# Performance work log

Hardware: AMD Instinct MI355X
Metric: run time of the kernel (lower is better)

## Reference

```python
import jax, jax.numpy as jnp
import numpy as np

B, C, N, K = 8, 3, 4096, 20
EPS = 1e-5

def bn(x, g, b, axes):
    # training-mode batch norm: normalize over batch/spatial axes, channel last
    m = jnp.mean(x, axes, keepdims=True)
    v = jnp.var(x, axes, keepdims=True)
    return g * (x - m) * jax.lax.rsqrt(v + EPS) + b

def setup_inputs() -> dict:
    key = jax.random.key(0)
    ks = jax.random.split(key, 8)
    def xav(kk, shape):
        fan_out, fan_in = shape
        lim = (6.0 / (fan_in + fan_out)) ** 0.5
        return jax.random.uniform(kk, shape, minval=-lim, maxval=lim, dtype=jnp.float32)
    return dict(
        x=jax.random.normal(ks[0], (B, C, N), dtype=jnp.float32),
        w1=xav(ks[1], (64, 2 * C)), g1=jnp.ones(64), b1=jnp.zeros(64),
        w2=xav(ks[2], (128, 64)), g2=jnp.ones(128), b2=jnp.zeros(128),
        w3=xav(ks[3], (1024, 128)), g3=jnp.ones(1024), b3=jnp.zeros(1024),
        w4=xav(ks[4], (512, 1024)), g4=jnp.ones(512), b4=jnp.zeros(512),
        w5=xav(ks[5], (256, 512)), g5=jnp.ones(256), b5=jnp.zeros(256),
        wl=jnp.zeros((9, 256), dtype=jnp.float32),  # zero-init per reset_parameters
        bl=jnp.zeros(9, dtype=jnp.float32),
    )

def reference(x, w1, g1, b1, w2, g2, b2, w3, g3, b3, w4, g4, b4, w5, g5, b5, wl, bl):
    xt = jnp.transpose(x, (0, 2, 1))  # (B, N, C)
    sq = jnp.sum(xt * xt, -1)  # (B, N)
    # negative squared pairwise distance: -(|a|^2 - 2ab + |b|^2)
    nd = 2.0 * jnp.einsum('bnc,bmc->bnm', xt, xt) - sq[:, :, None] - sq[:, None, :]
    _, idx = jax.lax.top_k(nd, K)  # (B, N, K) nearest neighbors (includes self)
    nbr = jax.vmap(lambda pts, ids: pts[ids])(xt, idx)  # (B, N, K, C)
    ctr = xt[:, :, None, :]
    edge = jnp.concatenate([jnp.broadcast_to(ctr, (B, N, K, C)), nbr - ctr], -1)  # (B,N,K,2C)
    # EdgeConv shared MLP (1x1 conv + BN + ReLU), then max over k
    h = jax.nn.relu(bn(jnp.einsum('bnkc,oc->bnko', edge, w1), g1, b1, (0, 1, 2)))
    h = jax.nn.relu(bn(jnp.einsum('bnkc,oc->bnko', h, w2), g2, b2, (0, 1, 2)))
    h = jnp.max(h, 2)  # (B, N, 128)
    # local shared MLP then global max pool over points
    h = jax.nn.relu(bn(jnp.einsum('bnc,oc->bno', h, w3), g3, b3, (0, 1)))
    h = jnp.max(h, 1)  # (B, 1024)
    # global MLP
    h = jax.nn.relu(bn(h @ w4.T, g4, b4, (0,)))
    h = jax.nn.relu(bn(h @ w5.T, g5, b5, (0,)))
    y = (h @ wl.T + bl).reshape(B, 3, 3)
    return y + jnp.eye(3, dtype=y.dtype)
```

## Files before the change

### kernel.cpp

```cpp
#include <hip/hip_runtime.h>

#define NPTS 4096
#define KNN 20
#define CNT1f 655360.0f
#define CNT3f 32768.0f
#define BNEPS 1e-5f

#define OFF_IDX   0
#define OFF_M     655360
#define OFF_ES    655360
#define OFF_G1P   656384
#define OFF_S1P   672768
#define ZERO1_BEG 655360
#define ZERO1_CNT 17664
#define OFF_W2B   2752512
#define OFF_W3B   2756608
#define OFF_XP    2822144
#define OFF_G3P   2953216
#define OFF_SM3P  2985984
#define OFF_GMAX  2986240
#define OFF_Z4    2994432
#define ZG3_BEG   2953216
#define ZG3_CNT   41216
#define OFF_SC1   4849664
#define OFF_SH1   4849728
#define OFF_SC2   4849792
#define OFF_SH2   4849920
#define OFF_SC3   4850048
#define OFF_SH3   4851072

typedef float f32x4 __attribute__((ext_vector_type(4)));
typedef short s16x8 __attribute__((ext_vector_type(8)));

__device__ __forceinline__ unsigned short f2bf(float f) {
    unsigned u = __float_as_uint(f);
    return (unsigned short)((u + 0x7FFFu + ((u >> 16) & 1u)) >> 16);
}

__global__ __launch_bounds__(256) void k_initprep(const float* __restrict__ x,
                                                  const float* __restrict__ w2,
                                                  const float* __restrict__ w3, float* W) {
    int i = blockIdx.x * 256 + threadIdx.x;
    unsigned short* w2b = (unsigned short*)(W + OFF_W2B);
    unsigned short* w3b = (unsigned short*)(W + OFF_W3B);
    w3b[i] = f2bf(w3[i]);
    if (i < 8192) w2b[i] = f2bf(w2[i]);
    if (i < ZERO1_CNT) W[ZERO1_BEG + i] = 0.0f;
    if (i < ZG3_CNT) W[ZG3_BEG + i] = 0.0f;
    if (i < 32768) {
        int b = i >> 12, j = i & 4095;
        float4 p;
        p.x = x[b * 12288 + j];
        p.y = x[b * 12288 + 4096 + j];
        p.z = x[b * 12288 + 8192 + j];
        p.w = 0.f;
        ((float4*)(W + OFF_XP))[i] = p;
    }
}

template <int PER>
__device__ __forceinline__ void wave_scan_find(const int* H, int K, int lane,
                                               int& B, int& below, int& hB) {
    int c[PER]; int s = 0;
    const int base = lane * PER;
#pragma unroll
    for (int p = 0; p < PER; ++p) { c[p] = H[base + p]; s += c[p]; }
    int pre = s;
#pragma unroll
    for (int off = 1; off < 64; off <<= 1) {
        int t = __shfl_up(pre, off, 64);
        if (lane >= off) pre += t;
    }
    int excl = pre - s;
    bool has = (excl < K) && (K <= excl + s);
    unsigned long long m = __ballot(has);
    int src = (int)(__ffsll((unsigned long long)m) - 1);
    int mb = 0, mbelow = 0, mh = 0;
    if (lane == src) {
        int cum = excl;
#pragma unroll
        for (int p = 0; p < PER; ++p) {
            if (cum < K && K <= cum + c[p]) { mb = base + p; mbelow = cum; mh = c[p]; break; }
            cum += c[p];
        }
    }
    B = __shfl(mb, src, 64);
    below = __shfl(mbelow, src, 64);
    hB = __shfl(mh, src, 64);
}

__global__ __launch_bounds__(256) void k_knn(int* __restrict__ idx, float* W) {
    __shared__ int hist[4][1024];
    __shared__ int outi[4][20];
    __shared__ int cnts[4][2];
    __shared__ float estat[27];
    const int tid = threadIdx.x;
    const int b = blockIdx.y;
    const float4* xb4 = ((const float4*)(W + OFF_XP)) + b * NPTS;
    if (tid < 27) estat[tid] = 0.f;
    if (tid < 8) cnts[tid >> 1][tid & 1] = 0;
    const int wv = tid >> 6, lane = tid & 63;
    const int q = blockIdx.x * 4 + wv;
    const float4 qp = xb4[q];
    int* H = hist[wv];
    unsigned int key[64];
    unsigned int mymin = 0xFFFFFFFFu;
#pragma unroll
    for (int p = 0; p < 16; ++p) H[lane * 16 + p] = 0;
#pragma unroll
    for (int it = 0; it < 64; ++it) {
        int j = it * 64 + lane;
        float4 pp = xb4[j];
        float dx = pp.x - qp.x, dy = pp.y - qp.y, dz = pp.z - qp.z;
        float d = fmaf(dx, dx, fmaf(dy, dy, dz * dz));
        unsigned int u = (j == q) ? 0xFFFFFFFFu : __float_as_uint(d);
        key[it] = u;
        mymin = mymin < u ? mymin : u;
    }
    __syncthreads();
#pragma unroll
    for (int off = 32; off; off >>= 1) {
        unsigned int o = (unsigned int)__shfl_xor((int)mymin, off);
        mymin = mymin < o ? mymin : o;
    }
    const unsigned int base = mymin;
#pragma unroll
    for (int it = 0; it < 64; ++it) {
        unsigned int t9 = key[it] - base;
        unsigned int bin = t9 >> 19; if (bin > 1023u) bin = 1023u;
        atomicAdd(&H[bin], 1);
    }
    int B, below, hB;
    wave_scan_find<16>(H, KNN - 1, lane, B, below, hB);
    unsigned int P = (unsigned int)B;
    int rem = (KNN - 1) - below;
    int S = 19;
    if (hB != rem) {
#pragma unroll
        for (int p = 0; p < 8; ++p) H[lane * 8 + p] = 0;
#pragma unroll
        for (int it = 0; it < 64; ++it) {
            unsigned int t9 = key[it] - base;
            unsigned int b0 = t9 >> 19; if (b0 > 1023u) b0 = 1023u;
            if (b0 == P) atomicAdd(&H[(t9 >> 10) & 511], 1);
        }
        wave_scan_find<8>(H, rem, lane, B, below, hB);
        P = (P << 9) | (unsigned int)B;
        rem -= below;
        S = 10;
        if (hB != rem) {
#pragma unroll
            for (int p = 0; p < 8; ++p) H[lane * 8 + p] = 0;
#pragma unroll
            for (int it = 0; it < 64; ++it) {
                unsigned int t9 = key[it] - base;
                if ((t9 >> 10) == P) atomicAdd(&H[(t9 >> 1) & 511], 1);
            }
            wave_scan_find<8>(H, rem, lane, B, below, hB);
            P = (P << 9) | (unsigned int)B;
            rem -= below;
            S = 1;
        }
    }
    int* OC = cnts[wv];
#pragma unroll
    for (int it = 0; it < 64; ++it) {
        unsigned int t9 = key[it] - base;
        unsigned int v;
        if (S == 19) { v = t9 >> 19; if (v > 1023u) v = 1023u; }
        else v = t9 >> S;
        if (v <= P) {
            bool take = v < P;
            if (!take) { int e = atomicAdd(&OC[1], 1); take = (e < rem); }
            if (take) { int pos = atomicAdd(&OC[0], 1); outi[wv][pos] = it * 64 + lane; }
        }
    }
    if (lane == 0) outi[wv][KNN - 1] = q;
    const int obase = (b * NPTS + q) * KNN;
    if (lane < KNN) idx[obase + lane] = outi[wv][lane];
    float st[27];
#pragma unroll
    for (int v = 0; v < 27; ++v) st[v] = 0.f;
    if (lane < KNN) {
        int j = outi[wv][lane];
        float4 np = xb4[j];
        float e[6];
        e[0] = qp.x; e[1] = qp.y; e[2] = qp.z;
        e[3] = np.x - qp.x; e[4] = np.y - qp.y; e[5] = np.z - qp.z;
        int id = 6;
#pragma unroll
        for (int i = 0; i < 6; ++i) {
            st[i] = e[i];
#pragma unroll
            for (int jj = i; jj < 6; ++jj) { st[id] = e[i] * e[jj]; id++; }
        }
    }
#pragma unroll
    for (int v = 0; v < 27; ++v) {
        float s = st[v];
        s += __shfl_xor(s, 32); s += __shfl_xor(s, 16); s += __shfl_xor(s, 8);
        s += __shfl_xor(s, 4);  s += __shfl_xor(s, 2);  s += __shfl_xor(s, 1);
        st[v] = s;
    }
    if (lane == 0) {
#pragma unroll
        for (int v = 0; v < 27; ++v) atomicAdd(&estat[v], st[v]);
    }
    __syncthreads();
    if (tid < 27) atomicAdd(&W[OFF_ES + (blockIdx.x & 31) * 32 + tid], estat[tid]);
}

__global__ void k_fin1(const float* __restrict__ w1, const float* __restrict__ g1,
                       const float* __restrict__ b1, float* W) {
    __shared__ float es[27];
    const int c = threadIdx.x;
    if (c < 27) {
        float s = 0.f;
        for (int p = 0; p < 32; ++p) s += W[OFF_ES + p * 32 + c];
        es[c] = s;
    }
    __syncthreads();
    float wr[6];
#pragma unroll
    for (int i = 0; i < 6; ++i) wr[i] = w1[c * 6 + i];
    float m = 0.f;
#pragma unroll
    for (int i = 0; i < 6; ++i) m += wr[i] * es[i];
    m *= (1.f / CNT1f);
    float qv = 0.f;
    int id = 6;
#pragma unroll
    for (int i = 0; i < 6; ++i)
#pragma unroll
        for (int jj = 0; jj < 6; ++jj)
            if (jj >= i) { qv += (jj == i ? 1.f : 2.f) * wr[i] * wr[jj] * es[id]; id++; }
    qv *= (1.f / CNT1f);
    float var = qv - m * m;
    float sc = g1[c] * rsqrtf(var + BNEPS);
    W[OFF_SC1 + c] = sc;
    W[OFF_SH1 + c] = b1[c] - m * sc;
}

__global__ __launch_bounds__(256) void k_gram1(const int* __restrict__ idx,
                                               const float* __restrict__ w1, float* W) {
    __shared__ unsigned short h1t[80 * 136];
    __shared__ float eds[128 * 6];
    __shared__ float w1s[64 * 6];
    __shared__ float sc1s[64], sh1s[64];
    const int t = threadIdx.x;
    const int b = blockIdx.x >> 6;
    const int ebase_b = (blockIdx.x & 63) * 1280;
    const float4* xpb = ((const float4*)(W + OFF_XP)) + b * NPTS;
    if (t < 384) w1s[t] = w1[t];
    if (t < 64) { sc1s[t] = W[OFF_SC1 + t]; sh1s[t] = W[OFF_SH1 + t]; }
    for (int i = t; i < 2048; i += 256) {
        int rr = i >> 7, e = i & 127;
        h1t[(64 + rr) * 136 + e] = (rr == 0) ? (unsigned short)0x3F80 : (unsigned short)0;
    }
    const int w = t >> 6, lane = t & 63, n16 = lane & 15, quad = lane >> 4;
    f32x4 acc[5];
#pragma unroll
    for (int j = 0; j < 5; ++j) acc[j] = (f32x4){0.f, 0.f, 0.f, 0.f};
    for (int ck = 0; ck < 10; ++ck) {
        __syncthreads();
        if (t < 128) {
            int e_l = ebase_b + ck * 128 + t;
            int q = e_l / KNN;
            int jn = idx[b * (NPTS * KNN) + e_l];
            float4 c = xpb[q];
            float4 n = xpb[jn];
            float* E = &eds[t * 6];
            E[0] = c.x; E[1] = c.y; E[2] = c.z;
            E[3] = n.x - c.x; E[4] = n.y - c.y; E[5] = n.z - c.z;
        }
        __syncthreads();
        {
            const int e128 = t & 127, half = t >> 7;
            float e0 = eds[e128 * 6 + 0], e1 = eds[e128 * 6 + 1], e2 = eds[e128 * 6 + 2];
            float e3 = eds[e128 * 6 + 3], e4 = eds[e128 * 6 + 4], e5 = eds[e128 * 6 + 5];
#pragma unroll 4
            for (int cc = 0; cc < 32; ++cc) {
                int c = half * 32 + cc;
                const float* wr = &w1s[c * 6];
                float z = wr[0] * e0 + wr[1] * e1 + wr[2] * e2 + wr[3] * e3 + wr[4] * e4 + wr[5] * e5;
                float h = sc1s[c] * z + sh1s[c];
                h1t[c * 136 + e128] = f2bf(h > 0.f ? h : 0.f);
            }
        }
        __syncthreads();
#pragma unroll
        for (int ks = 0; ks < 4; ++ks) {
            s16x8 Af = *(const s16x8*)&h1t[(w * 16 + n16) * 136 + ks * 32 + quad * 8];
#pragma unroll
            for (int jt = 0; jt < 5; ++jt) {
                s16x8 Bf = *(const s16x8*)&h1t[(jt * 16 + n16) * 136 + ks * 32 + quad * 8];
                acc[jt] = __builtin_amdgcn_mfma_f32_16x16x32_bf16(Af, Bf, acc[jt], 0, 0, 0);
            }
        }
    }
    const int part = blockIdx.x & 3;
    const int gi = w * 16 + quad * 4;
#pragma unroll
    for (int jt = 0; jt < 4; ++jt)
#pragma unroll
        for (int r = 0; r < 4; ++r)
            atomicAdd(&W[OFF_G1P + part * 4096 + (gi + r) * 64 + jt * 16 + n16], acc[jt][r]);
    if (n16 == 0) {
#pragma unroll
        for (int r = 0; r < 4; ++r)
            atomicAdd(&W[OFF_S1P + part * 64 + gi + r], acc[4][r]);
    }
}

__global__ __launch_bounds__(256) void k_fin2(const float* __restrict__ w2, const float* __restrict__ g2,
                                              const float* __restrict__ b2, float* W) {
    __shared__ float Gs[4096];
    __shared__ float s1s[64];
    __shared__ float w2s[128 * 65];
    const int t = threadIdx.x;
    for (int i = t; i < 4096; i += 256)
        Gs[i] = W[OFF_G1P + i] + W[OFF_G1P + 4096 + i] + W[OFF_G1P + 8192 + i] + W[OFF_G1P + 12288 + i];
    if (t < 64) s1s[t] = W[OFF_S1P + t] + W[OFF_S1P + 64 + t] + W[OFF_S1P + 128 + t] + W[OFF_S1P + 192 + t];
    for (int i = t; i < 8192; i += 256) w2s[(i >> 6) * 65 + (i & 63)] = w2[i];
    __syncthreads();
    const int c = t >> 1, half = t & 1;
    float acc = 0.f;
    for (int ii = 0; ii < 32; ++ii) {
        int i = 32 * half + ii;
        float wi = w2s[c * 65 + i];
        float inner = 0.f;
        for (int j = 0; j < 64; ++j) inner += Gs[i * 64 + j] * w2s[c * 65 + j];
        acc += wi * inner;
    }
    acc += __shfl_xor(acc, 1);
    if (half == 0) {
        float ms = 0.f;
        for (int j = 0; j < 64; ++j) ms += w2s[c * 65 + j] * s1s[j];
        float mean = ms * (1.f / CNT1f);
        float var = acc * (1.f / CNT1f) - mean * mean;
        float sc = g2[c] * rsqrtf(var + BNEPS);
        W[OFF_SC2 + c] = sc;
        W[OFF_SH2 + c] = b2[c] - mean * sc;
    }
}

__global__ __launch_bounds__(256) void k_c2apply(const int* __restrict__ idx,
                                                 const float* __restrict__ w1, float* W) {
    __shared__ unsigned short h1b[256 * 72];
    __shared__ float eds[160 * 6];
    const int t = threadIdx.x;
    const int b = blockIdx.y, q0 = blockIdx.x * 8;
    const float4* xpb = ((const float4*)(W + OFF_XP)) + b * NPTS;
    const int ebase = (b * NPTS + q0) * KNN;
    const unsigned short* w2b = (const unsigned short*)(W + OFF_W2B);
    if (t < 160) {
        int q = q0 + t / KNN;
        int jn = idx[ebase + t];
        float4 c = xpb[q];
        float4 n = xpb[jn];
        float* E = &eds[t * 6];
        E[0] = c.x; E[1] = c.y; E[2] = c.z;
        E[3] = n.x - c.x; E[4] = n.y - c.y; E[5] = n.z - c.z;
    }
    __syncthreads();
    {
        const int j64 = t & 63, grp = t >> 6;
        float wr[6];
#pragma unroll
        for (int i = 0; i < 6; ++i) wr[i] = w1[j64 * 6 + i];
        const float sc = W[OFF_SC1 + j64], sh = W[OFF_SH1 + j64];
        for (int qq = grp * 2; qq < grp * 2 + 2; ++qq) {
#pragma unroll 4
            for (int kk = 0; kk < 32; ++kk) {
                float v = 0.f;
                if (kk < 20) {
                    const float* E = &eds[(qq * 20 + kk) * 6];
                    float z = wr[0] * E[0] + wr[1] * E[1] + wr[2] * E[2] + wr[3] * E[3] + wr[4] * E[4] + wr[5] * E[5];
                    float h = sc * z + sh;
                    v = h > 0.f ? h : 0.f;
                }
                h1b[(qq * 32 + kk) * 72 + j64] = f2bf(v);
            }
        }
    }
    __syncthreads();
    const int w = t >> 6, lane = t & 63, n16 = lane & 15, quad = lane >> 4;
    unsigned short* Mb = (unsigned short*)(W + OFF_M);
#pragma unroll
    for (int nt_i = 0; nt_i < 2; ++nt_i) {
        const int nt = 2 * w + nt_i;
        const int chan = nt * 16 + n16;
        const float sc2 = W[OFF_SC2 + chan], sh2 = W[OFF_SH2 + chan];
        s16x8 Bf0 = *(const s16x8*)&w2b[chan * 64 + quad * 8];
        s16x8 Bf1 = *(const s16x8*)&w2b[chan * 64 + 32 + quad * 8];
#pragma unroll
        for (int q = 0; q < 8; ++q) {
            f32x4 accA = (f32x4){0.f, 0.f, 0.f, 0.f};
            f32x4 accB = (f32x4){0.f, 0.f, 0.f, 0.f};
            s16x8 a0 = *(const s16x8*)&h1b[(q * 32 + n16) * 72 + quad * 8];
            s16x8 a1 = *(const s16x8*)&h1b[(q * 32 + 16 + n16) * 72 + quad * 8];
            accA = __builtin_amdgcn_mfma_f32_16x16x32_bf16(a0, Bf0, accA, 0, 0, 0);
            accB = __builtin_amdgcn_mfma_f32_16x16x32_bf16(a1, Bf0, accB, 0, 0, 0);
            a0 = *(const s16x8*)&h1b[(q * 32 + n16) * 72 + 32 + quad * 8];
            a1 = *(const s16x8*)&h1b[(q * 32 + 16 + n16) * 72 + 32 + quad * 8];
            accA = __builtin_amdgcn_mfma_f32_16x16x32_bf16(a0, Bf1, accA, 0, 0, 0);
            accB = __builtin_amdgcn_mfma_f32_16x16x32_bf16(a1, Bf1, accB, 0, 0, 0);
            float mx = 0.f;
#pragma unroll
            for (int r = 0; r < 4; ++r) {
                float h = sc2 * accA[r] + sh2;
                mx = fmaxf(mx, h > 0.f ? h : 0.f);
            }
            if (quad == 0) {
#pragma unroll
                for (int r = 0; r < 4; ++r) {
                    float h = sc2 * accB[r] + sh2;
                    mx = fmaxf(mx, h > 0.f ? h : 0.f);
                }
            }
            mx = fmaxf(mx, __shfl_xor(mx, 16));
            mx = fmaxf(mx, __shfl_xor(mx, 32));
            if (quad == 0)
                Mb[(b * NPTS + q0 + q) * 128 + chan] = f2bf(mx);
        }
    }
}

__global__ __launch_bounds__(256) void k_gram3(float* W) {
    __shared__ unsigned short Mt[128 * 72];
    const int t = threadIdx.x;
    const int w = t >> 6, lane = t & 63, n16 = lane & 15, quad = lane >> 4;
    const int r0 = blockIdx.x * 512;
    const unsigned int* Msrc = (const unsigned int*)(W + OFF_M);
    const int nA = 8 - w;
    f32x4 acc[9];
#pragma unroll
    for (int j = 0; j < 9; ++j) acc[j] = (f32x4){0.f, 0.f, 0.f, 0.f};
    float smacc = 0.f;
    for (int ch = 0; ch < 8; ++ch) {
        __syncthreads();
        for (int i = t; i < 4096; i += 256) {
            int row = i >> 6, c2 = i & 63;
            unsigned int v = Msrc[(r0 + ch * 64 + row) * 64 + c2];
            Mt[(2 * c2) * 72 + row]     = (unsigned short)(v & 0xFFFFu);
            Mt[(2 * c2 + 1) * 72 + row] = (unsigned short)(v >> 16);
        }
        __syncthreads();
#pragma unroll
        for (int j = 0; j < 9; ++j) {
            int ti = (j < nA) ? w : (7 - w);
            int tj = (j < nA) ? (w + j) : (j - nA + 7 - w);
#pragma unroll
            for (int ks = 0; ks < 2; ++ks) {
                s16x8 Af = *(const s16x8*)&Mt[(ti * 16 + n16) * 72 + ks * 32 + quad * 8];
                s16x8 Bf = *(const s16x8*)&Mt[(tj * 16 + n16) * 72 + ks * 32 + quad * 8];
                acc[j] = __builtin_amdgcn_mfma_f32_16x16x32_bf16(Af, Bf, acc[j], 0, 0, 0);
            }
        }
        if (t < 128) {
            float s = 0.f;
            for (int e = 0; e < 64; ++e)
                s += __uint_as_float((unsigned int)Mt[t * 72 + e] << 16);
            smacc += s;
        }
    }
    const int part = blockIdx.x & 1;
    float* Gp = &W[OFF_G3P + part * 16384];
#pragma unroll
    for (int j = 0; j < 9; ++j) {
        int ti = (j < nA) ? w : (7 - w);
        int tj = (j < nA) ? (w + j) : (j - nA + 7 - w);
#pragma unroll
        for (int r = 0; r < 4; ++r)
            atomicAdd(&Gp[(ti * 16 + quad * 4 + r) * 128 + tj * 16 + n16], acc[j][r]);
    }
    if (t < 128) atomicAdd(&W[OFF_SM3P + part * 128 + t], smacc);
}

__global__ __launch_bounds__(256) void k_fin3(const float* __restrict__ w3, const float* __restrict__ g3,
                                              const float* __restrict__ b3, float* W) {
    __shared__ float G3s[128 * 129];
    __shared__ float w3s[16 * 132];
    __shared__ float sm3[128];
    __shared__ float red[256];
    __shared__ float mred[16];
    const int t = threadIdx.x;
    const int c0 = blockIdx.x * 16;
    for (int i = t; i < 16384; i += 256) {
        int row = i >> 7, col = i & 127;
        int src = ((row >> 4) <= (col >> 4)) ? (row * 128 + col) : (col * 128 + row);
        G3s[row * 129 + col] = W[OFF_G3P + src] + W[OFF_G3P + 16384 + src];
    }
    for (int i = t; i < 2048; i += 256)
        w3s[(i >> 7) * 132 + (i & 127)] = w3[(c0 + (i >> 7)) * 128 + (i & 127)];
    if (t < 128) sm3[t] = W[OFF_SM3P + t] + W[OFF_SM3P + 128 + t];
    __syncthreads();
    const int cl = t >> 4, seg = t & 15;
    float acc = 0.f;
    for (int ii = 0; ii < 8; ++ii) {
        int i = 8 * seg + ii;
        float wi = w3s[cl * 132 + i];
        float inner = 0.f;
        for (int j = 0; j < 128; ++j) inner += G3s[i * 129 + j] * w3s[cl * 132 + j];
        acc += wi * inner;
    }
    red[t] = acc;
    if (seg == 0) {
        float ms = 0.f;
        for (int j = 0; j < 128; ++j) ms += w3s[cl * 132 + j] * sm3[j];
        mred[cl] = ms;
    }
    __syncthreads();
    if (t < 16) {
        float s = 0.f;
#pragma unroll
        for (int k = 0; k < 16; ++k) s += red[t * 16 + k];
        float mean = mred[t] * (1.f / CNT3f);
        float var = s * (1.f / CNT3f) - mean * mean;
        float sc = g3[c0 + t] * rsqrtf(var + BNEPS);
        W[OFF_SC3 + c0 + t] = sc;
        W[OFF_SH3 + c0 + t] = b3[c0 + t] - mean * sc;
    }
}

__global__ __launch_bounds__(256) void k_conv3(float* W) {
    __shared__ unsigned short Mt[64 * 136];
    const int t = threadIdx.x;
    const int p0 = blockIdx.x * 64, c0g = blockIdx.y * 128;
    const unsigned int* Msrc = (const unsigned int*)(W + OFF_M);
    const unsigned short* w3b = (const unsigned short*)(W + OFF_W3B);
    for (int i = t; i < 4096; i += 256) {
        int row = i >> 6, c2 = i & 63;
        *(unsigned int*)&Mt[row * 136 + 2 * c2] = Msrc[(p0 + row) * 64 + c2];
    }
    __syncthreads();
    const int w = t >> 6, lane = t & 63, n16 = lane & 15, quad = lane >> 4;
    const int bbatch = p0 >> 12;
#pragma unroll
    for (int nt_i = 0; nt_i < 2; ++nt_i) {
        const int nt = 2 * w + nt_i;
        const int chan = c0g + nt * 16 + n16;
        const float sc3 = W[OFF_SC3 + chan], sh3 = W[OFF_SH3 + chan];
        s16x8 Bf[4];
#pragma unroll
        for (int ks = 0; ks < 4; ++ks)
            Bf[ks] = *(const s16x8*)&w3b[chan * 128 + ks * 32 + quad * 8];
        float mx = 0.f;
#pragma unroll
        for (int mt = 0; mt < 4; ++mt) {
            f32x4 acc = (f32x4){0.f, 0.f, 0.f, 0.f};
#pragma unroll
            for (int ks = 0; ks < 4; ++ks) {
                s16x8 Af = *(const s16x8*)&Mt[(mt * 16 + n16) * 136 + ks * 32 + quad * 8];
                acc = __builtin_amdgcn_mfma_f32_16x16x32_bf16(Af, Bf[ks], acc, 0, 0, 0);
            }
#pragma unroll
            for (int r = 0; r < 4; ++r) {
                float h = sc3 * acc[r] + sh3;
                mx = fmaxf(mx, h > 0.f ? h : 0.f);
            }
        }
        mx = fmaxf(mx, __shfl_xor(mx, 16));
        mx = fmaxf(mx, __shfl_xor(mx, 32));
        if (quad == 0)
            atomicMax((unsigned int*)&W[OFF_GMAX + bbatch * 1024 + chan], __float_as_uint(mx));
    }
}

__global__ __launch_bounds__(256) void k_fc4(const float* __restrict__ w4, float* W) {
    __shared__ float red[256];
    const int t = threadIdx.x;
    const int oidx = t >> 3, s = t & 7;
    const int cc = oidx >> 3, b = oidx & 7;
    const int c = blockIdx.x * 4 + cc;
    const float* g = &W[OFF_GMAX];
    const float* wr = &w4[c * 1024 + s * 128];
    const float* gr = &g[b * 1024 + s * 128];
    float p = 0.f;
    for (int j = 0; j < 128; ++j) p += wr[j] * gr[j];
    red[t] = p;
    __syncthreads();
    if (t < 32) {
        float tot = 0.f;
        for (int k = 0; k < 8; ++k) tot += red[t * 8 + k];
        W[OFF_Z4 + (t & 7) * 512 + blockIdx.x * 4 + (t >> 3)] = tot;
    }
}

__global__ __launch_bounds__(512) void k_tail(const float* __restrict__ g4, const float* __restrict__ b4,
                                              const float* __restrict__ w5, const float* __restrict__ g5,
                                              const float* __restrict__ b5, const float* __restrict__ wl,
                                              const float* __restrict__ bl, float* W, float* __restrict__ out) {
    __shared__ float h4L[8 * 512];
    __shared__ float w5s[2 * 256 * 9];
    __shared__ float zp[2 * 2048];
    const int t = threadIdx.x;
    {
        float v[8]; float s = 0.f, q = 0.f;
#pragma unroll
        for (int b = 0; b < 8; ++b) { v[b] = W[OFF_Z4 + b * 512 + t]; s += v[b]; q += v[b] * v[b]; }
        float mean = s * 0.125f;
        float var = q * 0.125f - mean * mean;
        float sc = g4[t] * rsqrtf(var + BNEPS);
        float sh = b4[t] - mean * sc;
#pragma unroll
        for (int b = 0; b < 8; ++b) {
            float h = sc * v[b] + sh;
            h4L[b * 512 + t] = h > 0.f ? h : 0.f;
        }
    }
    const int c5 = t & 255, half = t >> 8;
    float acc[8];
#pragma unroll
    for (int b = 0; b < 8; ++b) acc[b] = 0.f;
    for (int jt = 0; jt < 32; ++jt) {
        __syncthreads();
        for (int i = t; i < 4096; i += 512) {
            int h = i >> 11, rem = i & 2047;
            int ci = rem >> 3, jj = rem & 7;
            w5s[h * 2304 + ci * 9 + jj] = w5[ci * 512 + h * 256 + jt * 8 + jj];
        }
        __syncthreads();
#pragma unroll
        for (int jj = 0; jj < 8; ++jj) {
            float wv = w5s[half * 2304 + c5 * 9 + jj];
            int jg = half * 256 + jt * 8 + jj;
#pragma unroll
            for (int b = 0; b < 8; ++b) acc[b] += wv * h4L[b * 512 + jg];
        }
    }
#pragma unroll
    for (int b = 0; b < 8; ++b) zp[half * 2048 + b * 256 + c5] = acc[b];
    __syncthreads();
    if (t < 256) {
        float v[8], s = 0.f, q = 0.f;
#pragma unroll
        for (int b = 0; b < 8; ++b) {
            v[b] = zp[b * 256 + t] + zp[2048 + b * 256 + t];
            s += v[b]; q += v[b] * v[b];
        }
        float mean = s * 0.125f, var = q * 0.125f - mean * mean;
        float sc = g5[t] * rsqrtf(var + BNEPS), sh = b5[t] - mean * sc;
#pragma unroll
        for (int b = 0; b < 8; ++b) { float h = sc * v[b] + sh; zp[b * 256 + t] = h > 0.f ? h : 0.f; }
    }
    __syncthreads();
    if (t < 72) {
        int b = t / 9, r = t % 9;
        float a = bl[r] + ((r == 0 || r == 4 || r == 8) ? 1.f : 0.f);
        for (int j = 0; j < 256; ++j) a += wl[r * 256 + j] * zp[b * 256 + j];
        out[b * 9 + r] = a;
    }
}

extern "C" void kernel_launch(void* const* d_in, const int* in_sizes, int n_in,
                              void* d_out, int out_size, void* d_ws, size_t ws_size,
                              hipStream_t stream) {
    const float* x  = (const float*)d_in[0];
    const float* w1 = (const float*)d_in[1];
    const float* g1 = (const float*)d_in[2];
    const float* b1 = (const float*)d_in[3];
    const float* w2 = (const float*)d_in[4];
    const float* g2 = (const float*)d_in[5];
    const float* b2 = (const float*)d_in[6];
    const float* w3 = (const float*)d_in[7];
    const float* g3 = (const float*)d_in[8];
    const float* b3 = (const float*)d_in[9];
    const float* w4 = (const float*)d_in[10];
    const float* g4 = (const float*)d_in[11];
    const float* b4 = (const float*)d_in[12];
    const float* w5 = (const float*)d_in[13];
    const float* g5 = (const float*)d_in[14];
    const float* b5 = (const float*)d_in[15];
    const float* wl = (const float*)d_in[16];
    const float* bl = (const float*)d_in[17];
    float* W = (float*)d_ws;
    int* idx = (int*)d_ws;
    float* out = (float*)d_out;

    k_initprep<<<dim3(512), dim3(256), 0, stream>>>(x, w2, w3, W);
    k_knn<<<dim3(1024, 8), dim3(256), 0, stream>>>(idx, W);
    k_fin1<<<dim3(1), dim3(64), 0, stream>>>(w1, g1, b1, W);
    k_gram1<<<dim3(512), dim3(256), 0, stream>>>(idx, w1, W);
    k_fin2<<<dim3(1), dim3(256), 0, stream>>>(w2, g2, b2, W);
    k_c2apply<<<dim3(512, 8), dim3(256), 0, stream>>>(idx, w1, W);
    k_gram3<<<dim3(64), dim3(256), 0, stream>>>(W);
    k_fin3<<<dim3(64), dim3(256), 0, stream>>>(w3, g3, b3, W);
    k_conv3<<<dim3(512, 8), dim3(256), 0, stream>>>(W);
    k_fc4<<<dim3(128), dim3(256), 0, stream>>>(w4, W);
    k_tail<<<dim3(1), dim3(512), 0, stream>>>(g4, b4, w5, g5, b5, wl, bl, W, out);
}
```

Measured before the change: 597.0 us.

## Split each kNN query across two waves to halve per-thread key registers

The kNN selection kernel now handles one query with two cooperating waves (128 threads) instead of one wave, so each thread holds 32 distance keys instead of 64. The grid doubles to keep the same number of queries. The radix-select histogram shrinks to 512 bins and always runs three passes with block barriers, dropping the old early exit. The goal is lower register pressure and higher occupancy, at the cost of extra __syncthreads, always doing all passes, and slightly coarser final key resolution for tie handling.

```diff
diff --git a/kernel.cpp b/kernel.cpp
--- a/kernel.cpp
+++ b/kernel.cpp
@@ -90,26 +90,29 @@
 }
 
 __global__ __launch_bounds__(256) void k_knn(int* __restrict__ idx, float* W) {
-    __shared__ int hist[4][1024];
-    __shared__ int outi[4][20];
-    __shared__ int cnts[4][2];
+    __shared__ int hist[2][512];
+    __shared__ int outi[2][20];
+    __shared__ int cnts[2][2];
+    __shared__ unsigned int minsh[2][2];
     __shared__ float estat[27];
     const int tid = threadIdx.x;
     const int b = blockIdx.y;
     const float4* xb4 = ((const float4*)(W + OFF_XP)) + b * NPTS;
     if (tid < 27) estat[tid] = 0.f;
-    if (tid < 8) cnts[tid >> 1][tid & 1] = 0;
+    if (tid < 4) cnts[tid >> 1][tid & 1] = 0;
     const int wv = tid >> 6, lane = tid & 63;
-    const int q = blockIdx.x * 4 + wv;
+    const int pair = wv >> 1, half = wv & 1;
+    const int tid128 = tid & 127;
+    const int q = blockIdx.x * 2 + pair;
     const float4 qp = xb4[q];
-    int* H = hist[wv];
-    unsigned int key[64];
+    int* H = hist[pair];
+#pragma unroll
+    for (int p = 0; p < 4; ++p) H[tid128 * 4 + p] = 0;
+    unsigned int key[32];
     unsigned int mymin = 0xFFFFFFFFu;
 #pragma unroll
-    for (int p = 0; p < 16; ++p) H[lane * 16 + p] = 0;
-#pragma unroll
-    for (int it = 0; it < 64; ++it) {
-        int j = it * 64 + lane;
+    for (int it = 0; it < 32; ++it) {
+        int j = it * 128 + tid128;
         float4 pp = xb4[j];
         float dx = pp.x - qp.x, dy = pp.y - qp.y, dz = pp.z - qp.z;
         float d = fmaf(dx, dx, fmaf(dy, dy, dz * dz));
@@ -117,72 +120,71 @@
         key[it] = u;
         mymin = mymin < u ? mymin : u;
     }
-    __syncthreads();
 #pragma unroll
     for (int off = 32; off; off >>= 1) {
         unsigned int o = (unsigned int)__shfl_xor((int)mymin, off);
         mymin = mymin < o ? mymin : o;
     }
-    const unsigned int base = mymin;
-#pragma unroll
-    for (int it = 0; it < 64; ++it) {
+    if (lane == 0) minsh[pair][half] = mymin;
+    __syncthreads();
+    const unsigned int base = minsh[pair][0] < minsh[pair][1] ? minsh[pair][0] : minsh[pair][1];
+#pragma unroll
+    for (int it = 0; it < 32; ++it) {
         unsigned int t9 = key[it] - base;
-        unsigned int bin = t9 >> 19; if (bin > 1023u) bin = 1023u;
+        unsigned int bin = t9 >> 20; if (bin > 511u) bin = 511u;
         atomicAdd(&H[bin], 1);
     }
+    __syncthreads();
     int B, below, hB;
-    wave_scan_find<16>(H, KNN - 1, lane, B, below, hB);
+    wave_scan_find<8>(H, KNN - 1, lane, B, below, hB);
     unsigned int P = (unsigned int)B;
     int rem = (KNN - 1) - below;
-    int S = 19;
-    if (hB != rem) {
-#pragma unroll
-        for (int p = 0; p < 8; ++p) H[lane * 8 + p] = 0;
-#pragma unroll
-        for (int it = 0; it < 64; ++it) {
-            unsigned int t9 = key[it] - base;
-            unsigned int b0 = t9 >> 19; if (b0 > 1023u) b0 = 1023u;
-            if (b0 == P) atomicAdd(&H[(t9 >> 10) & 511], 1);
-        }
-        wave_scan_find<8>(H, rem, lane, B, below, hB);
-        P = (P << 9) | (unsigned int)B;
-        rem -= below;
-        S = 10;
-        if (hB != rem) {
-#pragma unroll
-            for (int p = 0; p < 8; ++p) H[lane * 8 + p] = 0;
-#pragma unroll
-            for (int it = 0; it < 64; ++it) {
-                unsigned int t9 = key[it] - base;
-                if ((t9 >> 10) == P) atomicAdd(&H[(t9 >> 1) & 511], 1);
-            }
-            wave_scan_find<8>(H, rem, lane, B, below, hB);
-            P = (P << 9) | (unsigned int)B;
-            rem -= below;
-            S = 1;
-        }
-    }
-    int* OC = cnts[wv];
-#pragma unroll
-    for (int it = 0; it < 64; ++it) {
+    __syncthreads();
+#pragma unroll
+    for (int p = 0; p < 4; ++p) H[tid128 * 4 + p] = 0;
+    __syncthreads();
+#pragma unroll
+    for (int it = 0; it < 32; ++it) {
         unsigned int t9 = key[it] - base;
-        unsigned int v;
-        if (S == 19) { v = t9 >> 19; if (v > 1023u) v = 1023u; }
-        else v = t9 >> S;
+        unsigned int b0 = t9 >> 20; if (b0 > 511u) b0 = 511u;
+        if (b0 == P) atomicAdd(&H[(t9 >> 11) & 511], 1);
+    }
+    __syncthreads();
+    wave_scan_find<8>(H, rem, lane, B, below, hB);
+    P = (P << 9) | (unsigned int)B;
+    rem -= below;
+    __syncthreads();
+#pragma unroll
+    for (int p = 0; p < 4; ++p) H[tid128 * 4 + p] = 0;
+    __syncthreads();
+#pragma unroll
+    for (int it = 0; it < 32; ++it) {
+        unsigned int t9 = key[it] - base;
+        if ((t9 >> 11) == P) atomicAdd(&H[(t9 >> 2) & 511], 1);
+    }
+    __syncthreads();
+    wave_scan_find<8>(H, rem, lane, B, below, hB);
+    P = (P << 9) | (unsigned int)B;
+    rem -= below;
+    int* OC = cnts[pair];
+#pragma unroll
+    for (int it = 0; it < 32; ++it) {
+        unsigned int v = (key[it] - base) >> 2;
         if (v <= P) {
             bool take = v < P;
             if (!take) { int e = atomicAdd(&OC[1], 1); take = (e < rem); }
-            if (take) { int pos = atomicAdd(&OC[0], 1); outi[wv][pos] = it * 64 + lane; }
-        }
-    }
-    if (lane == 0) outi[wv][KNN - 1] = q;
+            if (take) { int pos = atomicAdd(&OC[0], 1); outi[pair][pos] = it * 128 + tid128; }
+        }
+    }
+    if (half == 0 && lane == 0) outi[pair][KNN - 1] = q;
+    __syncthreads();
     const int obase = (b * NPTS + q) * KNN;
-    if (lane < KNN) idx[obase + lane] = outi[wv][lane];
+    if (half == 0 && lane < KNN) idx[obase + lane] = outi[pair][lane];
     float st[27];
 #pragma unroll
     for (int v = 0; v < 27; ++v) st[v] = 0.f;
-    if (lane < KNN) {
-        int j = outi[wv][lane];
+    if (half == 0 && lane < KNN) {
+        int j = outi[pair][lane];
         float4 np = xb4[j];
         float e[6];
         e[0] = qp.x; e[1] = qp.y; e[2] = qp.z;
@@ -195,16 +197,18 @@
             for (int jj = i; jj < 6; ++jj) { st[id] = e[i] * e[jj]; id++; }
         }
     }
-#pragma unroll
-    for (int v = 0; v < 27; ++v) {
-        float s = st[v];
-        s += __shfl_xor(s, 32); s += __shfl_xor(s, 16); s += __shfl_xor(s, 8);
-        s += __shfl_xor(s, 4);  s += __shfl_xor(s, 2);  s += __shfl_xor(s, 1);
-        st[v] = s;
-    }
-    if (lane == 0) {
-#pragma unroll
-        for (int v = 0; v < 27; ++v) atomicAdd(&estat[v], st[v]);
+    if (half == 0) {
+#pragma unroll
+        for (int v = 0; v < 27; ++v) {
+            float s = st[v];
+            s += __shfl_xor(s, 32); s += __shfl_xor(s, 16); s += __shfl_xor(s, 8);
+            s += __shfl_xor(s, 4);  s += __shfl_xor(s, 2);  s += __shfl_xor(s, 1);
+            st[v] = s;
+        }
+        if (lane == 0) {
+#pragma unroll
+            for (int v = 0; v < 27; ++v) atomicAdd(&estat[v], st[v]);
+        }
     }
     __syncthreads();
     if (tid < 27) atomicAdd(&W[OFF_ES + (blockIdx.x & 31) * 32 + tid], estat[tid]);
@@ -679,7 +683,7 @@
     float* out = (float*)d_out;
 
     k_initprep<<<dim3(512), dim3(256), 0, stream>>>(x, w2, w3, W);
-    k_knn<<<dim3(1024, 8), dim3(256), 0, stream>>>(idx, W);
+    k_knn<<<dim3(2048, 8), dim3(256), 0, stream>>>(idx, W);
     k_fin1<<<dim3(1), dim3(64), 0, stream>>>(w1, g1, b1, W);
     k_gram1<<<dim3(512), dim3(256), 0, stream>>>(idx, w1, W);
     k_fin2<<<dim3(1), dim3(256), 0, stream>>>(w2, g2, b2, W);
```

New measurement: 637.7 us. 6.8% more time.

## Compute conv1 via bf16 MFMA and split FC5 tail across blocks

Applied to the files above, without the earlier changes.

The first edge-conv layer (6->64) in k_gram1 and k_c2apply now runs as a bf16 MFMA on edge features zero-padded to 32, with w1 pre-converted to bf16 in the init kernel, instead of scalar FMA loops. The single-block k_tail is split into three kernels: a BN4 finalize, a 64-block FC5 matvec, and a small BN5 plus output kernel. This targets ALU time in the layer-1 recompute and the serial single-block FC5. It adds bf16 rounding on the raw edge coordinates and weights, plus two extra kernel launches.

```diff
diff --git a/kernel.cpp b/kernel.cpp
--- a/kernel.cpp
+++ b/kernel.cpp
@@ -28,6 +28,9 @@
 #define OFF_SH2   4849920
 #define OFF_SC3   4850048
 #define OFF_SH3   4851072
+#define OFF_H4    4852096
+#define OFF_Z5    4856192
+#define OFF_W1B   4858240
 
 typedef float f32x4 __attribute__((ext_vector_type(4)));
 typedef short s16x8 __attribute__((ext_vector_type(8)));
@@ -38,13 +41,19 @@
 }
 
 __global__ __launch_bounds__(256) void k_initprep(const float* __restrict__ x,
+                                                  const float* __restrict__ w1,
                                                   const float* __restrict__ w2,
                                                   const float* __restrict__ w3, float* W) {
     int i = blockIdx.x * 256 + threadIdx.x;
+    unsigned short* w1b = (unsigned short*)(W + OFF_W1B);
     unsigned short* w2b = (unsigned short*)(W + OFF_W2B);
     unsigned short* w3b = (unsigned short*)(W + OFF_W3B);
     w3b[i] = f2bf(w3[i]);
     if (i < 8192) w2b[i] = f2bf(w2[i]);
+    if (i < 2048) {
+        int c = i >> 5, k = i & 31;
+        w1b[i] = (k < 6) ? f2bf(w1[c * 6 + k]) : (unsigned short)0;
+    }
     if (i < ZERO1_CNT) W[ZERO1_BEG + i] = 0.0f;
     if (i < ZG3_CNT) W[ZG3_BEG + i] = 0.0f;
     if (i < 32768) {
@@ -241,23 +250,25 @@
     W[OFF_SH1 + c] = b1[c] - m * sc;
 }
 
-__global__ __launch_bounds__(256) void k_gram1(const int* __restrict__ idx,
-                                               const float* __restrict__ w1, float* W) {
+__global__ __launch_bounds__(256) void k_gram1(const int* __restrict__ idx, float* W) {
     __shared__ unsigned short h1t[80 * 136];
-    __shared__ float eds[128 * 6];
-    __shared__ float w1s[64 * 6];
+    __shared__ unsigned short eda[128 * 32];
     __shared__ float sc1s[64], sh1s[64];
     const int t = threadIdx.x;
     const int b = blockIdx.x >> 6;
     const int ebase_b = (blockIdx.x & 63) * 1280;
     const float4* xpb = ((const float4*)(W + OFF_XP)) + b * NPTS;
-    if (t < 384) w1s[t] = w1[t];
+    const unsigned short* w1b = (const unsigned short*)(W + OFF_W1B);
     if (t < 64) { sc1s[t] = W[OFF_SC1 + t]; sh1s[t] = W[OFF_SH1 + t]; }
     for (int i = t; i < 2048; i += 256) {
         int rr = i >> 7, e = i & 127;
         h1t[(64 + rr) * 136 + e] = (rr == 0) ? (unsigned short)0x3F80 : (unsigned short)0;
     }
     const int w = t >> 6, lane = t & 63, n16 = lane & 15, quad = lane >> 4;
+    s16x8 Bw1[4];
+#pragma unroll
+    for (int nt = 0; nt < 4; ++nt)
+        Bw1[nt] = *(const s16x8*)&w1b[(nt * 16 + n16) * 32 + quad * 8];
     f32x4 acc[5];
 #pragma unroll
     for (int j = 0; j < 5; ++j) acc[j] = (f32x4){0.f, 0.f, 0.f, 0.f};
@@ -269,22 +280,31 @@
             int jn = idx[b * (NPTS * KNN) + e_l];
             float4 c = xpb[q];
             float4 n = xpb[jn];
-            float* E = &eds[t * 6];
+            float E[6];
             E[0] = c.x; E[1] = c.y; E[2] = c.z;
             E[3] = n.x - c.x; E[4] = n.y - c.y; E[5] = n.z - c.z;
+            unsigned short* row = &eda[t * 32];
+#pragma unroll
+            for (int k = 0; k < 6; ++k) row[k] = f2bf(E[k]);
+#pragma unroll
+            for (int k = 6; k < 32; ++k) row[k] = 0;
         }
         __syncthreads();
-        {
-            const int e128 = t & 127, half = t >> 7;
-            float e0 = eds[e128 * 6 + 0], e1 = eds[e128 * 6 + 1], e2 = eds[e128 * 6 + 2];
-            float e3 = eds[e128 * 6 + 3], e4 = eds[e128 * 6 + 4], e5 = eds[e128 * 6 + 5];
-#pragma unroll 4
-            for (int cc = 0; cc < 32; ++cc) {
-                int c = half * 32 + cc;
-                const float* wr = &w1s[c * 6];
-                float z = wr[0] * e0 + wr[1] * e1 + wr[2] * e2 + wr[3] * e3 + wr[4] * e4 + wr[5] * e5;
-                float h = sc1s[c] * z + sh1s[c];
-                h1t[c * 136 + e128] = f2bf(h > 0.f ? h : 0.f);
+#pragma unroll
+        for (int i2 = 0; i2 < 2; ++i2) {
+            int tt = w + 4 * i2;
+            s16x8 Af = *(const s16x8*)&eda[(tt * 16 + n16) * 32 + quad * 8];
+#pragma unroll
+            for (int nt = 0; nt < 4; ++nt) {
+                f32x4 z = (f32x4){0.f, 0.f, 0.f, 0.f};
+                z = __builtin_amdgcn_mfma_f32_16x16x32_bf16(Af, Bw1[nt], z, 0, 0, 0);
+                int chan = nt * 16 + n16;
+                float sc = sc1s[chan], sh = sh1s[chan];
+#pragma unroll
+                for (int r = 0; r < 4; ++r) {
+                    float h = sc * z[r] + sh;
+                    h1t[chan * 136 + tt * 16 + quad * 4 + r] = f2bf(h > 0.f ? h : 0.f);
+                }
             }
         }
         __syncthreads();
@@ -344,47 +364,58 @@
     }
 }
 
-__global__ __launch_bounds__(256) void k_c2apply(const int* __restrict__ idx,
-                                                 const float* __restrict__ w1, float* W) {
+__global__ __launch_bounds__(256) void k_c2apply(const int* __restrict__ idx, float* W) {
     __shared__ unsigned short h1b[256 * 72];
-    __shared__ float eds[160 * 6];
+    __shared__ unsigned short eda[160 * 32];
+    __shared__ float sc1s[64], sh1s[64];
     const int t = threadIdx.x;
     const int b = blockIdx.y, q0 = blockIdx.x * 8;
     const float4* xpb = ((const float4*)(W + OFF_XP)) + b * NPTS;
     const int ebase = (b * NPTS + q0) * KNN;
     const unsigned short* w2b = (const unsigned short*)(W + OFF_W2B);
+    const unsigned short* w1b = (const unsigned short*)(W + OFF_W1B);
+    if (t < 64) { sc1s[t] = W[OFF_SC1 + t]; sh1s[t] = W[OFF_SH1 + t]; }
     if (t < 160) {
         int q = q0 + t / KNN;
         int jn = idx[ebase + t];
         float4 c = xpb[q];
         float4 n = xpb[jn];
-        float* E = &eds[t * 6];
+        float E[6];
         E[0] = c.x; E[1] = c.y; E[2] = c.z;
         E[3] = n.x - c.x; E[4] = n.y - c.y; E[5] = n.z - c.z;
-    }
-    __syncthreads();
-    {
-        const int j64 = t & 63, grp = t >> 6;
-        float wr[6];
-#pragma unroll
-        for (int i = 0; i < 6; ++i) wr[i] = w1[j64 * 6 + i];
-        const float sc = W[OFF_SC1 + j64], sh = W[OFF_SH1 + j64];
-        for (int qq = grp * 2; qq < grp * 2 + 2; ++qq) {
-#pragma unroll 4
-            for (int kk = 0; kk < 32; ++kk) {
-                float v = 0.f;
-                if (kk < 20) {
-                    const float* E = &eds[(qq * 20 + kk) * 6];
-                    float z = wr[0] * E[0] + wr[1] * E[1] + wr[2] * E[2] + wr[3] * E[3] + wr[4] * E[4] + wr[5] * E[5];
-                    float h = sc * z + sh;
-                    v = h > 0.f ? h : 0.f;
-                }
-                h1b[(qq * 32 + kk) * 72 + j64] = f2bf(v);
-            }
-        }
-    }
-    __syncthreads();
+        unsigned short* row = &eda[t * 32];
+#pragma unroll
+        for (int k = 0; k < 6; ++k) row[k] = f2bf(E[k]);
+#pragma unroll
+        for (int k = 6; k < 32; ++k) row[k] = 0;
+    }
     const int w = t >> 6, lane = t & 63, n16 = lane & 15, quad = lane >> 4;
+    s16x8 Bw1[4];
+#pragma unroll
+    for (int nt = 0; nt < 4; ++nt)
+        Bw1[nt] = *(const s16x8*)&w1b[(nt * 16 + n16) * 32 + quad * 8];
+    __syncthreads();
+#pragma unroll
+    for (int i2 = 0; i2 < 4; ++i2) {
+        int tt = w + 4 * i2;
+        int row = tt * 16 + n16;
+        int q = row >> 5, kk = row & 31;
+        s16x8 Af = (s16x8){0, 0, 0, 0, 0, 0, 0, 0};
+        if (kk < 20) Af = *(const s16x8*)&eda[(q * 20 + kk) * 32 + quad * 8];
+#pragma unroll
+        for (int nt = 0; nt < 4; ++nt) {
+            f32x4 z = (f32x4){0.f, 0.f, 0.f, 0.f};
+            z = __builtin_amdgcn_mfma_f32_16x16x32_bf16(Af, Bw1[nt], z, 0, 0, 0);
+            int chan = nt * 16 + n16;
+            float sc = sc1s[chan], sh = sh1s[chan];
+#pragma unroll
+            for (int r = 0; r < 4; ++r) {
+                float h = sc * z[r] + sh;
+                h1b[(tt * 16 + quad * 4 + r) * 72 + chan] = f2bf(h > 0.f ? h : 0.f);
+            }
+        }
+    }
+    __syncthreads();
     unsigned short* Mb = (unsigned short*)(W + OFF_M);
 #pragma unroll
     for (int nt_i = 0; nt_i < 2; ++nt_i) {
@@ -587,56 +618,52 @@
     }
 }
 
-__global__ __launch_bounds__(512) void k_tail(const float* __restrict__ g4, const float* __restrict__ b4,
-                                              const float* __restrict__ w5, const float* __restrict__ g5,
-                                              const float* __restrict__ b5, const float* __restrict__ wl,
-                                              const float* __restrict__ bl, float* W, float* __restrict__ out) {
-    __shared__ float h4L[8 * 512];
-    __shared__ float w5s[2 * 256 * 9];
-    __shared__ float zp[2 * 2048];
+__global__ __launch_bounds__(512) void k_fin4(const float* __restrict__ g4, const float* __restrict__ b4,
+                                              float* W) {
+    const int t = threadIdx.x;
+    float v[8]; float s = 0.f, q = 0.f;
+#pragma unroll
+    for (int b = 0; b < 8; ++b) { v[b] = W[OFF_Z4 + b * 512 + t]; s += v[b]; q += v[b] * v[b]; }
+    float mean = s * 0.125f;
+    float var = q * 0.125f - mean * mean;
+    float sc = g4[t] * rsqrtf(var + BNEPS);
+    float sh = b4[t] - mean * sc;
+#pragma unroll
+    for (int b = 0; b < 8; ++b) {
+        float h = sc * v[b] + sh;
+        W[OFF_H4 + b * 512 + t] = h > 0.f ? h : 0.f;
+    }
+}
+
+__global__ __launch_bounds__(256) void k_fc5(const float* __restrict__ w5, float* W) {
+    __shared__ float red[256];
+    const int t = threadIdx.x;
+    const int c4 = t >> 6, b = (t >> 3) & 7, s = t & 7;
+    const int c = blockIdx.x * 4 + c4;
+    const float* wr = &w5[c * 512 + s * 64];
+    const float* hr = &W[OFF_H4 + b * 512 + s * 64];
+    float p = 0.f;
+    for (int j = 0; j < 64; ++j) p += wr[j] * hr[j];
+    red[t] = p;
+    __syncthreads();
+    if (t < 32) {
+        const int cc = t >> 3, bb = t & 7;
+        float tot = 0.f;
+        for (int k = 0; k < 8; ++k) tot += red[cc * 64 + bb * 8 + k];
+        W[OFF_Z5 + bb * 256 + blockIdx.x * 4 + cc] = tot;
+    }
+}
+
+__global__ __launch_bounds__(256) void k_tail2(const float* __restrict__ g5, const float* __restrict__ b5,
+                                               const float* __restrict__ wl, const float* __restrict__ bl,
+                                               float* W, float* __restrict__ out) {
+    __shared__ float zp[2048];
     const int t = threadIdx.x;
     {
-        float v[8]; float s = 0.f, q = 0.f;
-#pragma unroll
-        for (int b = 0; b < 8; ++b) { v[b] = W[OFF_Z4 + b * 512 + t]; s += v[b]; q += v[b] * v[b]; }
-        float mean = s * 0.125f;
-        float var = q * 0.125f - mean * mean;
-        float sc = g4[t] * rsqrtf(var + BNEPS);
-        float sh = b4[t] - mean * sc;
+        float v[8], s = 0.f, q = 0.f;
 #pragma unroll
         for (int b = 0; b < 8; ++b) {
-            float h = sc * v[b] + sh;
-            h4L[b * 512 + t] = h > 0.f ? h : 0.f;
-        }
-    }
-    const int c5 = t & 255, half = t >> 8;
-    float acc[8];
-#pragma unroll
-    for (int b = 0; b < 8; ++b) acc[b] = 0.f;
-    for (int jt = 0; jt < 32; ++jt) {
-        __syncthreads();
-        for (int i = t; i < 4096; i += 512) {
-            int h = i >> 11, rem = i & 2047;
-            int ci = rem >> 3, jj = rem & 7;
-            w5s[h * 2304 + ci * 9 + jj] = w5[ci * 512 + h * 256 + jt * 8 + jj];
-        }
-        __syncthreads();
-#pragma unroll
-        for (int jj = 0; jj < 8; ++jj) {
-            float wv = w5s[half * 2304 + c5 * 9 + jj];
-            int jg = half * 256 + jt * 8 + jj;
-#pragma unroll
-            for (int b = 0; b < 8; ++b) acc[b] += wv * h4L[b * 512 + jg];
-        }
-    }
-#pragma unroll
-    for (int b = 0; b < 8; ++b) zp[half * 2048 + b * 256 + c5] = acc[b];
-    __syncthreads();
-    if (t < 256) {
-        float v[8], s = 0.f, q = 0.f;
-#pragma unroll
-        for (int b = 0; b < 8; ++b) {
-            v[b] = zp[b * 256 + t] + zp[2048 + b * 256 + t];
+            v[b] = W[OFF_Z5 + b * 256 + t];
             s += v[b]; q += v[b] * v[b];
         }
         float mean = s * 0.125f, var = q * 0.125f - mean * mean;
@@ -678,15 +705,17 @@
     int* idx = (int*)d_ws;
     float* out = (float*)d_out;
 
-    k_initprep<<<dim3(512), dim3(256), 0, stream>>>(x, w2, w3, W);
+    k_initprep<<<dim3(512), dim3(256), 0, stream>>>(x, w1, w2, w3, W);
     k_knn<<<dim3(1024, 8), dim3(256), 0, stream>>>(idx, W);
     k_fin1<<<dim3(1), dim3(64), 0, stream>>>(w1, g1, b1, W);
-    k_gram1<<<dim3(512), dim3(256), 0, stream>>>(idx, w1, W);
+    k_gram1<<<dim3(512), dim3(256), 0, stream>>>(idx, W);
     k_fin2<<<dim3(1), dim3(256), 0, stream>>>(w2, g2, b2, W);
-    k_c2apply<<<dim3(512, 8), dim3(256), 0, stream>>>(idx, w1, W);
+    k_c2apply<<<dim3(512, 8), dim3(256), 0, stream>>>(idx, W);
     k_gram3<<<dim3(64), dim3(256), 0, stream>>>(W);
     k_fin3<<<dim3(64), dim3(256), 0, stream>>>(w3, g3, b3, W);
     k_conv3<<<dim3(512, 8), dim3(256), 0, stream>>>(W);
     k_fc4<<<dim3(128), dim3(256), 0, stream>>>(w4, W);
-    k_tail<<<dim3(1), dim3(512), 0, stream>>>(g4, b4, w5, g5, b5, wl, bl, W, out);
-}
+    k_fin4<<<dim3(1), dim3(512), 0, stream>>>(g4, b4, W);
+    k_fc5<<<dim3(64), dim3(256), 0, stream>>>(w5, W);
+    k_tail2<<<dim3(1), dim3(256), 0, stream>>>(g5, b5, wl, bl, W, out);
+}
```

Result: faster. 524.1 us (-12.2%).
